# Performance work log

Measured on AMD Instinct MI355X. Metric: run time of the kernel, lower is better.

## Reference

```python
import jax, jax.numpy as jnp
import numpy as np

HEADS = 12
FEATURES = 768
D_HEAD = FEATURES // HEADS
SCALE = float(np.sqrt(D_HEAD))
EPS = 1e-12
N = 2048


def setup_inputs() -> dict:
    key = jax.random.key(0)
    ks = jax.random.split(key, 5)
    init = 1.0 / np.sqrt(FEATURES)
    return {
        "x": jax.random.normal(ks[0], (N, FEATURES), dtype=jnp.float32),
        "Wq": jax.random.normal(ks[1], (FEATURES, FEATURES), dtype=jnp.float32) * init,
        "Wk": jax.random.normal(ks[2], (FEATURES, FEATURES), dtype=jnp.float32) * init,
        "Wv": jax.random.normal(ks[3], (FEATURES, FEATURES), dtype=jnp.float32) * init,
        "Wo": jax.random.normal(ks[4], (FEATURES, FEATURES), dtype=jnp.float32) * init,
        "gamma": jnp.ones((FEATURES,), dtype=jnp.float32),
        "beta": jnp.zeros((FEATURES,), dtype=jnp.float32),
    }


def reference(x, Wq, Wk, Wv, Wo, gamma, beta):
    n = x.shape[0]
    # projections (no bias); weight layout [out, in] -> x @ W.T
    q = (x @ Wq.T).reshape(n, HEADS, D_HEAD).transpose(1, 0, 2)  # [h, n, d]
    k = (x @ Wk.T).reshape(n, HEADS, D_HEAD).transpose(1, 0, 2)
    v = (x @ Wv.T).reshape(n, HEADS, D_HEAD).transpose(1, 0, 2)
    # scores [h, n, n]; original divides q@k^T by sqrt(d_head)
    att = jnp.einsum("hnd,hmd->hnm", q, k) / SCALE
    att = jax.nn.softmax(att, axis=-1)  # dropout p=0 -> identity
    out = jnp.einsum("hnm,hmd->hnd", att, v)  # [h, n, d]
    out = out.transpose(1, 0, 2).reshape(n, FEATURES)  # n (h d)
    out = out @ Wo.T
    # residual + layernorm (eps=1e-12)
    y = out + x
    mu = jnp.mean(y, axis=-1, keepdims=True)
    var = jnp.mean((y - mu) ** 2, axis=-1, keepdims=True)
    return (y - mu) / jnp.sqrt(var + EPS) * gamma + beta
```

## Files before the change

### kernel.cpp

```cpp
#include <hip/hip_runtime.h>
#include <hip/hip_bf16.h>
#include <math.h>

#define N_TOK 2048
#define FEAT  768
#define HEADS 12
#define DHEAD 64
#define SPLIT 4
#define KV_PER (N_TOK / SPLIT)

typedef __bf16 v8bf __attribute__((ext_vector_type(8)));
typedef __bf16 v4bf __attribute__((ext_vector_type(4)));
typedef float  v4f  __attribute__((ext_vector_type(4)));

#define XE ((size_t)N_TOK * FEAT)
#define WE ((size_t)FEAT * FEAT)
#define QK_LD 1536

#define SCALE_FOLD 0.18033688011112042f

__device__ __forceinline__ void gload16(const __bf16* g, __bf16* l) {
    __builtin_amdgcn_global_load_lds(
        (const __attribute__((address_space(1))) unsigned int*)g,
        (__attribute__((address_space(3))) unsigned int*)l, 16, 0, 0);
}

__global__ __launch_bounds__(256) void cvt_all(
        const float* __restrict__ x,  const float* __restrict__ Wq,
        const float* __restrict__ Wk, const float* __restrict__ Wv,
        const float* __restrict__ Wo,
        __bf16* __restrict__ xb, __bf16* __restrict__ wqkv, __bf16* __restrict__ wob) {
    size_t i = ((size_t)blockIdx.x * 256 + threadIdx.x) * 4;
    const float* src; __bf16* dst; size_t off; float scale = 1.f;
    if (i < XE)               { src = x;  dst = xb;          off = i; }
    else if (i < XE + WE)     { src = Wq; dst = wqkv;        off = i - XE; scale = SCALE_FOLD; }
    else if (i < XE + 2 * WE) { src = Wk; dst = wqkv + WE;   off = i - XE - WE; }
    else if (i < XE + 3 * WE) { src = Wv; dst = wqkv + 2*WE; off = i - XE - 2*WE; }
    else                      { src = Wo; dst = wob;         off = i - XE - 3*WE; }
    float4 v = *(const float4*)(src + off);
    v4bf o;
    o[0] = (__bf16)(v.x * scale); o[1] = (__bf16)(v.y * scale);
    o[2] = (__bf16)(v.z * scale); o[3] = (__bf16)(v.w * scale);
    *(v4bf*)(dst + off) = o;
}

__global__ __launch_bounds__(256) void gemm_qkv(
        const __bf16* __restrict__ A, const __bf16* __restrict__ B,
        __bf16* __restrict__ qk, __bf16* __restrict__ vt) {
    __shared__ __bf16 As[64][32];
    __shared__ __bf16 Bs[128][32];
    const int t    = threadIdx.x;
    const int lane = t & 63, w = t >> 6;
    const int quad = lane >> 4, l15 = lane & 15;
    const int wm = w & 1, wn = w >> 1;
    const int bm = blockIdx.y * 64, bn = blockIdx.x * 128;
    const int srow = lane >> 2, scol = (lane & 3) * 8;

    v4f acc[2][4] = {};
    for (int k0 = 0; k0 < FEAT; k0 += 32) {
        gload16(A + (size_t)(bm + w * 16 + srow) * FEAT + k0 + scol,      &As[w * 16][0]);
        gload16(B + (size_t)(bn + w * 32 + srow) * FEAT + k0 + scol,      &Bs[w * 32][0]);
        gload16(B + (size_t)(bn + w * 32 + 16 + srow) * FEAT + k0 + scol, &Bs[w * 32 + 16][0]);
        __syncthreads();
        v8bf a[2], b[4];
#pragma unroll
        for (int mi = 0; mi < 2; mi++) a[mi] = *(const v8bf*)&As[wm * 32 + mi * 16 + l15][quad * 8];
#pragma unroll
        for (int ni = 0; ni < 4; ni++) b[ni] = *(const v8bf*)&Bs[wn * 64 + ni * 16 + l15][quad * 8];
#pragma unroll
        for (int mi = 0; mi < 2; mi++)
#pragma unroll
            for (int ni = 0; ni < 4; ni++)
                acc[mi][ni] = __builtin_amdgcn_mfma_f32_16x16x32_bf16(a[mi], b[ni], acc[mi][ni], 0, 0, 0);
        __syncthreads();
    }
    if (bn < 2 * FEAT) {
#pragma unroll
        for (int mi = 0; mi < 2; mi++)
#pragma unroll
            for (int ni = 0; ni < 4; ni++) {
                int col = bn + wn * 64 + ni * 16 + l15;
#pragma unroll
                for (int r = 0; r < 4; r++) {
                    int row = bm + wm * 32 + mi * 16 + quad * 4 + r;
                    qk[(size_t)row * QK_LD + col] = (__bf16)acc[mi][ni][r];
                }
            }
    } else {
#pragma unroll
        for (int mi = 0; mi < 2; mi++)
#pragma unroll
            for (int ni = 0; ni < 4; ni++) {
                int col = bn + wn * 64 + ni * 16 + l15 - 2 * FEAT;
                int row = bm + wm * 32 + mi * 16 + quad * 4;
                v4bf pk;
#pragma unroll
                for (int r = 0; r < 4; r++) pk[r] = (__bf16)acc[mi][ni][r];
                *(v4bf*)(vt + (size_t)col * N_TOK + row) = pk;
            }
    }
}

__global__ __launch_bounds__(256, 3) void attention(
        const __bf16* __restrict__ QK, const __bf16* __restrict__ vt,
        __bf16* __restrict__ Opart, float* __restrict__ lpart) {
    __shared__ __bf16 KV[2][2][64][64];
    __shared__ __bf16 P[4][32][68];
    const int t    = threadIdx.x;
    const int lane = t & 63, w = t >> 6;
    const int quad = lane >> 4, l15 = lane & 15;
    const int h = blockIdx.y, s = blockIdx.z;
    const int q0 = blockIdx.x * 128 + w * 32;

    v8bf qf[2][2];
#pragma unroll
    for (int mh = 0; mh < 2; mh++) {
        const __bf16* qp = QK + (size_t)(q0 + mh * 16 + l15) * QK_LD + h * DHEAD + quad * 8;
        qf[mh][0] = *(const v8bf*)qp;
        qf[mh][1] = *(const v8bf*)(qp + 32);
    }
    const __bf16* kg = QK + FEAT + h * DHEAD;
    const __bf16* vg = vt + (size_t)(h * DHEAD) * N_TOK;

    v4f o_acc[2][4] = {};
    float lacc[2][4] = {{0.f,0.f,0.f,0.f},{0.f,0.f,0.f,0.f}};

    const int kvbeg = s * KV_PER;
    const int lr8 = lane >> 3;

    auto stage = [&](int b, int kv0) {
#pragma unroll
        for (int i = 0; i < 2; i++) {
            int row = w * 16 + i * 8 + lr8;
            int gs  = (lane & 7) ^ (row & 7);
            gload16(kg + (size_t)(kv0 + row) * QK_LD + gs * 8, &KV[b][0][w * 16 + i * 8][0]);
            gload16(vg + (size_t)row * N_TOK + kv0 + gs * 8,   &KV[b][1][w * 16 + i * 8][0]);
        }
    };

    auto step = [&](int b) {
        v8bf kf[4][2];
#pragma unroll
        for (int nt = 0; nt < 4; nt++)
#pragma unroll
            for (int ks = 0; ks < 2; ks++)
                kf[nt][ks] = *(const v8bf*)&KV[b][0][nt * 16 + l15][((ks * 4 + quad) ^ (l15 & 7)) * 8];
        v4f sv[2][4];
#pragma unroll
        for (int mh = 0; mh < 2; mh++)
#pragma unroll
            for (int nt = 0; nt < 4; nt++) {
                v4f a = {};
                a = __builtin_amdgcn_mfma_f32_16x16x32_bf16(qf[mh][0], kf[nt][0], a, 0, 0, 0);
                a = __builtin_amdgcn_mfma_f32_16x16x32_bf16(qf[mh][1], kf[nt][1], a, 0, 0, 0);
                sv[mh][nt] = a;
            }
#pragma unroll
        for (int mh = 0; mh < 2; mh++)
#pragma unroll
            for (int r = 0; r < 4; r++) {
                float p0 = __builtin_amdgcn_exp2f(sv[mh][0][r]);
                float p1 = __builtin_amdgcn_exp2f(sv[mh][1][r]);
                float p2 = __builtin_amdgcn_exp2f(sv[mh][2][r]);
                float p3 = __builtin_amdgcn_exp2f(sv[mh][3][r]);
                lacc[mh][r] += (p0 + p1) + (p2 + p3);
                P[w][mh * 16 + quad * 4 + r][ 0 + l15] = (__bf16)p0;
                P[w][mh * 16 + quad * 4 + r][16 + l15] = (__bf16)p1;
                P[w][mh * 16 + quad * 4 + r][32 + l15] = (__bf16)p2;
                P[w][mh * 16 + quad * 4 + r][48 + l15] = (__bf16)p3;
            }
        v8bf vf[2][4];
#pragma unroll
        for (int ks = 0; ks < 2; ks++)
#pragma unroll
            for (int dt = 0; dt < 4; dt++)
                vf[ks][dt] = *(const v8bf*)&KV[b][1][dt * 16 + l15][((ks * 4 + quad) ^ (l15 & 7)) * 8];
#pragma unroll
        for (int mh = 0; mh < 2; mh++)
#pragma unroll
            for (int ks = 0; ks < 2; ks++) {
                v8bf pa = *(const v8bf*)&P[w][mh * 16 + l15][ks * 32 + quad * 8];
#pragma unroll
                for (int dt = 0; dt < 4; dt++)
                    o_acc[mh][dt] = __builtin_amdgcn_mfma_f32_16x16x32_bf16(pa, vf[ks][dt], o_acc[mh][dt], 0, 0, 0);
            }
    };

    stage(0, kvbeg);
    const int TILES = KV_PER / 64;
    for (int tt = 0; tt < TILES; tt++) {
        __syncthreads();
        if (tt + 1 < TILES) stage((tt + 1) & 1, kvbeg + (tt + 1) * 64);
        step(tt & 1);
    }

    __bf16* op = Opart + (size_t)s * XE;
#pragma unroll
    for (int mh = 0; mh < 2; mh++)
#pragma unroll
        for (int r = 0; r < 4; r++) {
            float l = lacc[mh][r];
            l += __shfl_xor(l, 1); l += __shfl_xor(l, 2);
            l += __shfl_xor(l, 4); l += __shfl_xor(l, 8);
            float linv = 1.0f / l;
            int row = q0 + mh * 16 + quad * 4 + r;
            if (l15 == 0) lpart[((size_t)s * HEADS + h) * N_TOK + row] = l;
#pragma unroll
            for (int dt = 0; dt < 4; dt++)
                op[(size_t)row * FEAT + h * DHEAD + dt * 16 + l15] = (__bf16)(o_acc[mh][dt][r] * linv);
        }
}

__global__ __launch_bounds__(256) void gemm_out(
        const __bf16* __restrict__ Op, const float* __restrict__ lp,
        const __bf16* __restrict__ Wo, const float* __restrict__ x,
        float* __restrict__ Yf) {
    __shared__ __bf16 As[64][32];
    __shared__ __bf16 Bs[128][32];
    const int t    = threadIdx.x;
    const int lane = t & 63, w = t >> 6;
    const int quad = lane >> 4, l15 = lane & 15;
    const int wm = w & 1, wn = w >> 1;
    const int bm = blockIdx.y * 64, bn = blockIdx.x * 128;
    const int srow = lane >> 2, scol = (lane & 3) * 8;

    const int ar = t >> 2, ac = (t & 3) * 8;
    const int arow = bm + ar;

    v4f acc[2][4] = {};
    for (int k0 = 0; k0 < FEAT; k0 += 32) {
        {
            int h = (k0 + ac) >> 6;
            float ls[SPLIT], tot = 0.f;
#pragma unroll
            for (int s = 0; s < SPLIT; s++) {
                ls[s] = lp[((size_t)s * HEADS + h) * N_TOK + arow];
                tot += ls[s];
            }
            float inv = 1.0f / tot;
            float a8[8] = {};
#pragma unroll
            for (int s = 0; s < SPLIT; s++) {
                v8bf p = *(const v8bf*)(Op + (size_t)s * XE + (size_t)arow * FEAT + k0 + ac);
                float wgt = ls[s] * inv;
#pragma unroll
                for (int j = 0; j < 8; j++) a8[j] += wgt * (float)p[j];
            }
            v8bf av;
#pragma unroll
            for (int j = 0; j < 8; j++) av[j] = (__bf16)a8[j];
            *(v8bf*)&As[ar][ac] = av;
        }
        gload16(Wo + (size_t)(bn + w * 32 + srow) * FEAT + k0 + scol,      &Bs[w * 32][0]);
        gload16(Wo + (size_t)(bn + w * 32 + 16 + srow) * FEAT + k0 + scol, &Bs[w * 32 + 16][0]);
        __syncthreads();
        v8bf a[2], b[4];
#pragma unroll
        for (int mi = 0; mi < 2; mi++) a[mi] = *(const v8bf*)&As[wm * 32 + mi * 16 + l15][quad * 8];
#pragma unroll
        for (int ni = 0; ni < 4; ni++) b[ni] = *(const v8bf*)&Bs[wn * 64 + ni * 16 + l15][quad * 8];
#pragma unroll
        for (int mi = 0; mi < 2; mi++)
#pragma unroll
            for (int ni = 0; ni < 4; ni++)
                acc[mi][ni] = __builtin_amdgcn_mfma_f32_16x16x32_bf16(a[mi], b[ni], acc[mi][ni], 0, 0, 0);
        __syncthreads();
    }
#pragma unroll
    for (int mi = 0; mi < 2; mi++)
#pragma unroll
        for (int ni = 0; ni < 4; ni++) {
            int col = bn + wn * 64 + ni * 16 + l15;
#pragma unroll
            for (int r = 0; r < 4; r++) {
                int row = bm + wm * 32 + mi * 16 + quad * 4 + r;
                Yf[(size_t)row * FEAT + col] = acc[mi][ni][r] + x[(size_t)row * FEAT + col];
            }
        }
}

__global__ __launch_bounds__(256) void ln_kernel(
        const float* __restrict__ Y, const float* __restrict__ gamma,
        const float* __restrict__ beta, float* __restrict__ out) {
    __shared__ float sbuf[4];
    const int row = blockIdx.x, t = threadIdx.x;
    const float* y = Y + (size_t)row * FEAT;
    float v0 = y[t], v1 = y[t + 256], v2 = y[t + 512];
    float s = v0 + v1 + v2;
#pragma unroll
    for (int m = 32; m; m >>= 1) s += __shfl_xor(s, m);
    if ((t & 63) == 0) sbuf[t >> 6] = s;
    __syncthreads();
    float mean = (sbuf[0] + sbuf[1] + sbuf[2] + sbuf[3]) * (1.f / FEAT);
    __syncthreads();
    float d0 = v0 - mean, d1 = v1 - mean, d2 = v2 - mean;
    float q = d0 * d0 + d1 * d1 + d2 * d2;
#pragma unroll
    for (int m = 32; m; m >>= 1) q += __shfl_xor(q, m);
    if ((t & 63) == 0) sbuf[t >> 6] = q;
    __syncthreads();
    float var = (sbuf[0] + sbuf[1] + sbuf[2] + sbuf[3]) * (1.f / FEAT);
    float rs = rsqrtf(var + 1e-12f);
    float* o = out + (size_t)row * FEAT;
    o[t]       = d0 * rs * gamma[t]       + beta[t];
    o[t + 256] = d1 * rs * gamma[t + 256] + beta[t + 256];
    o[t + 512] = d2 * rs * gamma[t + 512] + beta[t + 512];
}

extern "C" void kernel_launch(void* const* d_in, const int* in_sizes, int n_in,
                              void* d_out, int out_size, void* d_ws, size_t ws_size,
                              hipStream_t stream) {
    const float* x     = (const float*)d_in[0];
    const float* Wq    = (const float*)d_in[1];
    const float* Wk    = (const float*)d_in[2];
    const float* Wv    = (const float*)d_in[3];
    const float* Wo    = (const float*)d_in[4];
    const float* gamma = (const float*)d_in[5];
    const float* beta  = (const float*)d_in[6];
    float* out = (float*)d_out;

    char* ws = (char*)d_ws;
    size_t off = 0;
    auto alloc = [&](size_t bytes) -> void* {
        void* p = ws + off;
        off += (bytes + 255) & ~(size_t)255;
        return p;
    };
    __bf16* xb   = (__bf16*)alloc(XE * 2);
    __bf16* wqkv = (__bf16*)alloc(3 * WE * 2);
    __bf16* wob  = (__bf16*)alloc(WE * 2);
    __bf16* qk   = (__bf16*)alloc((size_t)N_TOK * QK_LD * 2);
    __bf16* vtb  = (__bf16*)alloc((size_t)FEAT * N_TOK * 2);
    __bf16* Op   = (__bf16*)alloc(SPLIT * XE * 2);
    float*  lp   = (float*)alloc(SPLIT * HEADS * N_TOK * 4);
    float*  Yf   = (float*)ws;

    cvt_all<<<(int)((XE + 4 * WE) / 4 / 256), 256, 0, stream>>>(x, Wq, Wk, Wv, Wo, xb, wqkv, wob);

    gemm_qkv<<<dim3((QK_LD + FEAT) / 128, N_TOK / 64), 256, 0, stream>>>(xb, wqkv, qk, vtb);

    attention<<<dim3(N_TOK / 128, HEADS, SPLIT), 256, 0, stream>>>(qk, vtb, Op, lp);

    gemm_out<<<dim3(FEAT / 128, N_TOK / 64), 256, 0, stream>>>(Op, lp, wob, x, Yf);

    ln_kernel<<<N_TOK, 256, 0, stream>>>(Yf, gamma, beta, out);
}
```

Before: 151.2 us.

## Transpose attention score MFMAs and enlarge QKV GEMM M-tile to 128

The attention kernel now computes S^T = K·Q^T and O^T = V^T·P^T. Each lane then holds four consecutive kv scores for one query, so P is written to LDS as packed 4-element vectors with an XOR swizzle rather than as scalar stores. The row-sum reduction shrinks to two cross-quad shuffles, and the output is stored as vectors. Separately, the QKV GEMM tile doubles to 128x128, raising reuse per LDS load at the cost of more accumulator registers and half as many blocks.

Result: no change. 151.2 us (-0.0%).

```diff
diff --git a/kernel.cpp b/kernel.cpp
--- a/kernel.cpp
+++ b/kernel.cpp
@@ -47,28 +47,29 @@
 __global__ __launch_bounds__(256) void gemm_qkv(
         const __bf16* __restrict__ A, const __bf16* __restrict__ B,
         __bf16* __restrict__ qk, __bf16* __restrict__ vt) {
-    __shared__ __bf16 As[64][32];
+    __shared__ __bf16 As[128][32];
     __shared__ __bf16 Bs[128][32];
     const int t    = threadIdx.x;
     const int lane = t & 63, w = t >> 6;
     const int quad = lane >> 4, l15 = lane & 15;
     const int wm = w & 1, wn = w >> 1;
-    const int bm = blockIdx.y * 64, bn = blockIdx.x * 128;
+    const int bm = blockIdx.y * 128, bn = blockIdx.x * 128;
     const int srow = lane >> 2, scol = (lane & 3) * 8;
 
-    v4f acc[2][4] = {};
+    v4f acc[4][4] = {};
     for (int k0 = 0; k0 < FEAT; k0 += 32) {
-        gload16(A + (size_t)(bm + w * 16 + srow) * FEAT + k0 + scol,      &As[w * 16][0]);
+        gload16(A + (size_t)(bm + w * 32 + srow) * FEAT + k0 + scol,      &As[w * 32][0]);
+        gload16(A + (size_t)(bm + w * 32 + 16 + srow) * FEAT + k0 + scol, &As[w * 32 + 16][0]);
         gload16(B + (size_t)(bn + w * 32 + srow) * FEAT + k0 + scol,      &Bs[w * 32][0]);
         gload16(B + (size_t)(bn + w * 32 + 16 + srow) * FEAT + k0 + scol, &Bs[w * 32 + 16][0]);
         __syncthreads();
-        v8bf a[2], b[4];
-#pragma unroll
-        for (int mi = 0; mi < 2; mi++) a[mi] = *(const v8bf*)&As[wm * 32 + mi * 16 + l15][quad * 8];
+        v8bf a[4], b[4];
+#pragma unroll
+        for (int mi = 0; mi < 4; mi++) a[mi] = *(const v8bf*)&As[wm * 64 + mi * 16 + l15][quad * 8];
 #pragma unroll
         for (int ni = 0; ni < 4; ni++) b[ni] = *(const v8bf*)&Bs[wn * 64 + ni * 16 + l15][quad * 8];
 #pragma unroll
-        for (int mi = 0; mi < 2; mi++)
+        for (int mi = 0; mi < 4; mi++)
 #pragma unroll
             for (int ni = 0; ni < 4; ni++)
                 acc[mi][ni] = __builtin_amdgcn_mfma_f32_16x16x32_bf16(a[mi], b[ni], acc[mi][ni], 0, 0, 0);
@@ -76,23 +77,23 @@
     }
     if (bn < 2 * FEAT) {
 #pragma unroll
-        for (int mi = 0; mi < 2; mi++)
+        for (int mi = 0; mi < 4; mi++)
 #pragma unroll
             for (int ni = 0; ni < 4; ni++) {
                 int col = bn + wn * 64 + ni * 16 + l15;
 #pragma unroll
                 for (int r = 0; r < 4; r++) {
-                    int row = bm + wm * 32 + mi * 16 + quad * 4 + r;
+                    int row = bm + wm * 64 + mi * 16 + quad * 4 + r;
                     qk[(size_t)row * QK_LD + col] = (__bf16)acc[mi][ni][r];
                 }
             }
     } else {
 #pragma unroll
-        for (int mi = 0; mi < 2; mi++)
+        for (int mi = 0; mi < 4; mi++)
 #pragma unroll
             for (int ni = 0; ni < 4; ni++) {
                 int col = bn + wn * 64 + ni * 16 + l15 - 2 * FEAT;
-                int row = bm + wm * 32 + mi * 16 + quad * 4;
+                int row = bm + wm * 64 + mi * 16 + quad * 4;
                 v4bf pk;
 #pragma unroll
                 for (int r = 0; r < 4; r++) pk[r] = (__bf16)acc[mi][ni][r];
@@ -105,25 +106,26 @@
         const __bf16* __restrict__ QK, const __bf16* __restrict__ vt,
         __bf16* __restrict__ Opart, float* __restrict__ lpart) {
     __shared__ __bf16 KV[2][2][64][64];
-    __shared__ __bf16 P[4][32][68];
+    __shared__ __bf16 PT[4][32][64];
     const int t    = threadIdx.x;
     const int lane = t & 63, w = t >> 6;
     const int quad = lane >> 4, l15 = lane & 15;
     const int h = blockIdx.y, s = blockIdx.z;
     const int q0 = blockIdx.x * 128 + w * 32;
+    const int sw = (l15 & 7) * 8;
 
     v8bf qf[2][2];
 #pragma unroll
-    for (int mh = 0; mh < 2; mh++) {
-        const __bf16* qp = QK + (size_t)(q0 + mh * 16 + l15) * QK_LD + h * DHEAD + quad * 8;
-        qf[mh][0] = *(const v8bf*)qp;
-        qf[mh][1] = *(const v8bf*)(qp + 32);
+    for (int qt = 0; qt < 2; qt++) {
+        const __bf16* qp = QK + (size_t)(q0 + qt * 16 + l15) * QK_LD + h * DHEAD + quad * 8;
+        qf[qt][0] = *(const v8bf*)qp;
+        qf[qt][1] = *(const v8bf*)(qp + 32);
     }
     const __bf16* kg = QK + FEAT + h * DHEAD;
     const __bf16* vg = vt + (size_t)(h * DHEAD) * N_TOK;
 
-    v4f o_acc[2][4] = {};
-    float lacc[2][4] = {{0.f,0.f,0.f,0.f},{0.f,0.f,0.f,0.f}};
+    v4f o_acc[4][2] = {};
+    float lacc[2] = {0.f, 0.f};
 
     const int kvbeg = s * KV_PER;
     const int lr8 = lane >> 3;
@@ -141,33 +143,32 @@
     auto step = [&](int b) {
         v8bf kf[4][2];
 #pragma unroll
-        for (int nt = 0; nt < 4; nt++)
+        for (int kvt = 0; kvt < 4; kvt++)
 #pragma unroll
             for (int ks = 0; ks < 2; ks++)
-                kf[nt][ks] = *(const v8bf*)&KV[b][0][nt * 16 + l15][((ks * 4 + quad) ^ (l15 & 7)) * 8];
-        v4f sv[2][4];
-#pragma unroll
-        for (int mh = 0; mh < 2; mh++)
-#pragma unroll
-            for (int nt = 0; nt < 4; nt++) {
+                kf[kvt][ks] = *(const v8bf*)&KV[b][0][kvt * 16 + l15][((ks * 4 + quad) ^ (l15 & 7)) * 8];
+        v4f sv[4][2];
+#pragma unroll
+        for (int kvt = 0; kvt < 4; kvt++)
+#pragma unroll
+            for (int qt = 0; qt < 2; qt++) {
                 v4f a = {};
-                a = __builtin_amdgcn_mfma_f32_16x16x32_bf16(qf[mh][0], kf[nt][0], a, 0, 0, 0);
-                a = __builtin_amdgcn_mfma_f32_16x16x32_bf16(qf[mh][1], kf[nt][1], a, 0, 0, 0);
-                sv[mh][nt] = a;
-            }
-#pragma unroll
-        for (int mh = 0; mh < 2; mh++)
-#pragma unroll
-            for (int r = 0; r < 4; r++) {
-                float p0 = __builtin_amdgcn_exp2f(sv[mh][0][r]);
-                float p1 = __builtin_amdgcn_exp2f(sv[mh][1][r]);
-                float p2 = __builtin_amdgcn_exp2f(sv[mh][2][r]);
-                float p3 = __builtin_amdgcn_exp2f(sv[mh][3][r]);
-                lacc[mh][r] += (p0 + p1) + (p2 + p3);
-                P[w][mh * 16 + quad * 4 + r][ 0 + l15] = (__bf16)p0;
-                P[w][mh * 16 + quad * 4 + r][16 + l15] = (__bf16)p1;
-                P[w][mh * 16 + quad * 4 + r][32 + l15] = (__bf16)p2;
-                P[w][mh * 16 + quad * 4 + r][48 + l15] = (__bf16)p3;
+                a = __builtin_amdgcn_mfma_f32_16x16x32_bf16(kf[kvt][0], qf[qt][0], a, 0, 0, 0);
+                a = __builtin_amdgcn_mfma_f32_16x16x32_bf16(kf[kvt][1], qf[qt][1], a, 0, 0, 0);
+                sv[kvt][qt] = a;
+            }
+#pragma unroll
+        for (int kvt = 0; kvt < 4; kvt++)
+#pragma unroll
+            for (int qt = 0; qt < 2; qt++) {
+                float p0 = __builtin_amdgcn_exp2f(sv[kvt][qt][0]);
+                float p1 = __builtin_amdgcn_exp2f(sv[kvt][qt][1]);
+                float p2 = __builtin_amdgcn_exp2f(sv[kvt][qt][2]);
+                float p3 = __builtin_amdgcn_exp2f(sv[kvt][qt][3]);
+                lacc[qt] += (p0 + p1) + (p2 + p3);
+                v4bf pk;
+                pk[0] = (__bf16)p0; pk[1] = (__bf16)p1; pk[2] = (__bf16)p2; pk[3] = (__bf16)p3;
+                *(v4bf*)&PT[w][qt * 16 + l15][(kvt * 16 + quad * 4) ^ sw] = pk;
             }
         v8bf vf[2][4];
 #pragma unroll
@@ -175,15 +176,19 @@
 #pragma unroll
             for (int dt = 0; dt < 4; dt++)
                 vf[ks][dt] = *(const v8bf*)&KV[b][1][dt * 16 + l15][((ks * 4 + quad) ^ (l15 & 7)) * 8];
-#pragma unroll
-        for (int mh = 0; mh < 2; mh++)
-#pragma unroll
-            for (int ks = 0; ks < 2; ks++) {
-                v8bf pa = *(const v8bf*)&P[w][mh * 16 + l15][ks * 32 + quad * 8];
-#pragma unroll
-                for (int dt = 0; dt < 4; dt++)
-                    o_acc[mh][dt] = __builtin_amdgcn_mfma_f32_16x16x32_bf16(pa, vf[ks][dt], o_acc[mh][dt], 0, 0, 0);
-            }
+        v8bf ptf[2][2];
+#pragma unroll
+        for (int ks = 0; ks < 2; ks++)
+#pragma unroll
+            for (int qt = 0; qt < 2; qt++)
+                ptf[ks][qt] = *(const v8bf*)&PT[w][qt * 16 + l15][(ks * 32 + quad * 8) ^ sw];
+#pragma unroll
+        for (int dt = 0; dt < 4; dt++)
+#pragma unroll
+            for (int ks = 0; ks < 2; ks++)
+#pragma unroll
+                for (int qt = 0; qt < 2; qt++)
+                    o_acc[dt][qt] = __builtin_amdgcn_mfma_f32_16x16x32_bf16(vf[ks][dt], ptf[ks][qt], o_acc[dt][qt], 0, 0, 0);
     };
 
     stage(0, kvbeg);
@@ -196,19 +201,20 @@
 
     __bf16* op = Opart + (size_t)s * XE;
 #pragma unroll
-    for (int mh = 0; mh < 2; mh++)
-#pragma unroll
-        for (int r = 0; r < 4; r++) {
-            float l = lacc[mh][r];
-            l += __shfl_xor(l, 1); l += __shfl_xor(l, 2);
-            l += __shfl_xor(l, 4); l += __shfl_xor(l, 8);
-            float linv = 1.0f / l;
-            int row = q0 + mh * 16 + quad * 4 + r;
-            if (l15 == 0) lpart[((size_t)s * HEADS + h) * N_TOK + row] = l;
-#pragma unroll
-            for (int dt = 0; dt < 4; dt++)
-                op[(size_t)row * FEAT + h * DHEAD + dt * 16 + l15] = (__bf16)(o_acc[mh][dt][r] * linv);
+    for (int qt = 0; qt < 2; qt++) {
+        float l = lacc[qt];
+        l += __shfl_xor(l, 16); l += __shfl_xor(l, 32);
+        float linv = 1.0f / l;
+        int q = q0 + qt * 16 + l15;
+        if (quad == 0) lpart[((size_t)s * HEADS + h) * N_TOK + q] = l;
+#pragma unroll
+        for (int dt = 0; dt < 4; dt++) {
+            v4bf pk;
+#pragma unroll
+            for (int r = 0; r < 4; r++) pk[r] = (__bf16)(o_acc[dt][qt][r] * linv);
+            *(v4bf*)(op + (size_t)q * FEAT + h * DHEAD + dt * 16 + quad * 4) = pk;
         }
+    }
 }
 
 __global__ __launch_bounds__(256) void gemm_out(
@@ -337,7 +343,7 @@
 
     cvt_all<<<(int)((XE + 4 * WE) / 4 / 256), 256, 0, stream>>>(x, Wq, Wk, Wv, Wo, xb, wqkv, wob);
 
-    gemm_qkv<<<dim3((QK_LD + FEAT) / 128, N_TOK / 64), 256, 0, stream>>>(xb, wqkv, qk, vtb);
+    gemm_qkv<<<dim3((QK_LD + FEAT) / 128, N_TOK / 128), 256, 0, stream>>>(xb, wqkv, qk, vtb);
 
     attention<<<dim3(N_TOK / 128, HEADS, SPLIT), 256, 0, stream>>>(qk, vtb, Op, lp);
 
```

## Transpose attention MFMA operands, widen per-wave query tile, double KV split

Applied to the files above, without the earlier changes.

The attention kernel now computes S^T = K·Q^T, so each lane holds four consecutive kv scores for one query. That allows packed 4-wide bf16 stores of P^T into a padded LDS buffer and computes O^T with V as the A operand. Each wave now covers 64 queries instead of 32, so every K/V tile staged in LDS is reused across twice as many queries. SPLIT goes from 4 to 8 so the grid stays the same size. The cost is more accumulator registers per wave and more partial outputs that gemm_out must merge.

New measurement: 197.4 us. 1.31x slower.

```diff
diff --git a/kernel.cpp b/kernel.cpp
--- a/kernel.cpp
+++ b/kernel.cpp
@@ -6,7 +6,7 @@
 #define FEAT  768
 #define HEADS 12
 #define DHEAD 64
-#define SPLIT 4
+#define SPLIT 8
 #define KV_PER (N_TOK / SPLIT)
 
 typedef __bf16 v8bf __attribute__((ext_vector_type(8)));
@@ -105,25 +105,25 @@
         const __bf16* __restrict__ QK, const __bf16* __restrict__ vt,
         __bf16* __restrict__ Opart, float* __restrict__ lpart) {
     __shared__ __bf16 KV[2][2][64][64];
-    __shared__ __bf16 P[4][32][68];
+    __shared__ __bf16 PT[4][64][40];
     const int t    = threadIdx.x;
     const int lane = t & 63, w = t >> 6;
     const int quad = lane >> 4, l15 = lane & 15;
     const int h = blockIdx.y, s = blockIdx.z;
-    const int q0 = blockIdx.x * 128 + w * 32;
-
-    v8bf qf[2][2];
-#pragma unroll
-    for (int mh = 0; mh < 2; mh++) {
-        const __bf16* qp = QK + (size_t)(q0 + mh * 16 + l15) * QK_LD + h * DHEAD + quad * 8;
-        qf[mh][0] = *(const v8bf*)qp;
-        qf[mh][1] = *(const v8bf*)(qp + 32);
+    const int q0 = blockIdx.x * 256 + w * 64;
+
+    v8bf qf[4][2];
+#pragma unroll
+    for (int qt = 0; qt < 4; qt++) {
+        const __bf16* qp = QK + (size_t)(q0 + qt * 16 + l15) * QK_LD + h * DHEAD + quad * 8;
+        qf[qt][0] = *(const v8bf*)qp;
+        qf[qt][1] = *(const v8bf*)(qp + 32);
     }
     const __bf16* kg = QK + FEAT + h * DHEAD;
     const __bf16* vg = vt + (size_t)(h * DHEAD) * N_TOK;
 
-    v4f o_acc[2][4] = {};
-    float lacc[2][4] = {{0.f,0.f,0.f,0.f},{0.f,0.f,0.f,0.f}};
+    v4f o_acc[4][4] = {};
+    float lacc[4] = {0.f, 0.f, 0.f, 0.f};
 
     const int kvbeg = s * KV_PER;
     const int lr8 = lane >> 3;
@@ -139,51 +139,41 @@
     };
 
     auto step = [&](int b) {
-        v8bf kf[4][2];
-#pragma unroll
-        for (int nt = 0; nt < 4; nt++)
-#pragma unroll
-            for (int ks = 0; ks < 2; ks++)
-                kf[nt][ks] = *(const v8bf*)&KV[b][0][nt * 16 + l15][((ks * 4 + quad) ^ (l15 & 7)) * 8];
-        v4f sv[2][4];
-#pragma unroll
-        for (int mh = 0; mh < 2; mh++)
-#pragma unroll
-            for (int nt = 0; nt < 4; nt++) {
-                v4f a = {};
-                a = __builtin_amdgcn_mfma_f32_16x16x32_bf16(qf[mh][0], kf[nt][0], a, 0, 0, 0);
-                a = __builtin_amdgcn_mfma_f32_16x16x32_bf16(qf[mh][1], kf[nt][1], a, 0, 0, 0);
-                sv[mh][nt] = a;
-            }
-#pragma unroll
-        for (int mh = 0; mh < 2; mh++)
-#pragma unroll
-            for (int r = 0; r < 4; r++) {
-                float p0 = __builtin_amdgcn_exp2f(sv[mh][0][r]);
-                float p1 = __builtin_amdgcn_exp2f(sv[mh][1][r]);
-                float p2 = __builtin_amdgcn_exp2f(sv[mh][2][r]);
-                float p3 = __builtin_amdgcn_exp2f(sv[mh][3][r]);
-                lacc[mh][r] += (p0 + p1) + (p2 + p3);
-                P[w][mh * 16 + quad * 4 + r][ 0 + l15] = (__bf16)p0;
-                P[w][mh * 16 + quad * 4 + r][16 + l15] = (__bf16)p1;
-                P[w][mh * 16 + quad * 4 + r][32 + l15] = (__bf16)p2;
-                P[w][mh * 16 + quad * 4 + r][48 + l15] = (__bf16)p3;
-            }
-        v8bf vf[2][4];
-#pragma unroll
-        for (int ks = 0; ks < 2; ks++)
+#pragma unroll
+        for (int half = 0; half < 2; half++) {
+#pragma unroll
+            for (int kk = 0; kk < 2; kk++) {
+                int kvt = half * 2 + kk;
+                v8bf kf0 = *(const v8bf*)&KV[b][0][kvt * 16 + l15][((0 + quad) ^ (l15 & 7)) * 8];
+                v8bf kf1 = *(const v8bf*)&KV[b][0][kvt * 16 + l15][((4 + quad) ^ (l15 & 7)) * 8];
+#pragma unroll
+                for (int qt = 0; qt < 4; qt++) {
+                    v4f a = {};
+                    a = __builtin_amdgcn_mfma_f32_16x16x32_bf16(kf0, qf[qt][0], a, 0, 0, 0);
+                    a = __builtin_amdgcn_mfma_f32_16x16x32_bf16(kf1, qf[qt][1], a, 0, 0, 0);
+                    float p0 = __builtin_amdgcn_exp2f(a[0]);
+                    float p1 = __builtin_amdgcn_exp2f(a[1]);
+                    float p2 = __builtin_amdgcn_exp2f(a[2]);
+                    float p3 = __builtin_amdgcn_exp2f(a[3]);
+                    lacc[qt] += (p0 + p1) + (p2 + p3);
+                    v4bf pk;
+                    pk[0] = (__bf16)p0; pk[1] = (__bf16)p1; pk[2] = (__bf16)p2; pk[3] = (__bf16)p3;
+                    *(v4bf*)&PT[w][qt * 16 + l15][kk * 16 + quad * 4] = pk;
+                }
+            }
+            v8bf vf[4], ptf[4];
 #pragma unroll
             for (int dt = 0; dt < 4; dt++)
-                vf[ks][dt] = *(const v8bf*)&KV[b][1][dt * 16 + l15][((ks * 4 + quad) ^ (l15 & 7)) * 8];
-#pragma unroll
-        for (int mh = 0; mh < 2; mh++)
-#pragma unroll
-            for (int ks = 0; ks < 2; ks++) {
-                v8bf pa = *(const v8bf*)&P[w][mh * 16 + l15][ks * 32 + quad * 8];
-#pragma unroll
-                for (int dt = 0; dt < 4; dt++)
-                    o_acc[mh][dt] = __builtin_amdgcn_mfma_f32_16x16x32_bf16(pa, vf[ks][dt], o_acc[mh][dt], 0, 0, 0);
-            }
+                vf[dt] = *(const v8bf*)&KV[b][1][dt * 16 + l15][((half * 4 + quad) ^ (l15 & 7)) * 8];
+#pragma unroll
+            for (int qt = 0; qt < 4; qt++)
+                ptf[qt] = *(const v8bf*)&PT[w][qt * 16 + l15][quad * 8];
+#pragma unroll
+            for (int dt = 0; dt < 4; dt++)
+#pragma unroll
+                for (int qt = 0; qt < 4; qt++)
+                    o_acc[dt][qt] = __builtin_amdgcn_mfma_f32_16x16x32_bf16(vf[dt], ptf[qt], o_acc[dt][qt], 0, 0, 0);
+        }
     };
 
     stage(0, kvbeg);
@@ -196,19 +186,20 @@
 
     __bf16* op = Opart + (size_t)s * XE;
 #pragma unroll
-    for (int mh = 0; mh < 2; mh++)
-#pragma unroll
-        for (int r = 0; r < 4; r++) {
-            float l = lacc[mh][r];
-            l += __shfl_xor(l, 1); l += __shfl_xor(l, 2);
-            l += __shfl_xor(l, 4); l += __shfl_xor(l, 8);
-            float linv = 1.0f / l;
-            int row = q0 + mh * 16 + quad * 4 + r;
-            if (l15 == 0) lpart[((size_t)s * HEADS + h) * N_TOK + row] = l;
-#pragma unroll
-            for (int dt = 0; dt < 4; dt++)
-                op[(size_t)row * FEAT + h * DHEAD + dt * 16 + l15] = (__bf16)(o_acc[mh][dt][r] * linv);
-        }
+    for (int qt = 0; qt < 4; qt++) {
+        float l = lacc[qt];
+        l += __shfl_xor(l, 16); l += __shfl_xor(l, 32);
+        float linv = 1.0f / l;
+        int q = q0 + qt * 16 + l15;
+        if (quad == 0) lpart[((size_t)s * HEADS + h) * N_TOK + q] = l;
+#pragma unroll
+        for (int dt = 0; dt < 4; dt++) {
+            v4bf pk;
+#pragma unroll
+            for (int r = 0; r < 4; r++) pk[r] = (__bf16)(o_acc[dt][qt][r] * linv);
+            *(v4bf*)(op + (size_t)q * FEAT + h * DHEAD + dt * 16 + quad * 4) = pk;
+        }
+    }
 }
 
 __global__ __launch_bounds__(256) void gemm_out(
@@ -339,7 +330,7 @@
 
     gemm_qkv<<<dim3((QK_LD + FEAT) / 128, N_TOK / 64), 256, 0, stream>>>(xb, wqkv, qk, vtb);
 
-    attention<<<dim3(N_TOK / 128, HEADS, SPLIT), 256, 0, stream>>>(qk, vtb, Op, lp);
+    attention<<<dim3(N_TOK / 256, HEADS, SPLIT), 256, 0, stream>>>(qk, vtb, Op, lp);
 
     gemm_out<<<dim3(FEAT / 128, N_TOK / 64), 256, 0, stream>>>(Op, lp, wob, x, Yf);
 
```
